# Kernel tuning notes

Measured on AMD Instinct MI355X. Metric: run time of the kernel, lower is better.

The kernel has to match this reference:

```python
import jax, jax.numpy as jnp
import numpy as np

EPS = 1e-8

def div_safe(n, d):
    return n / jnp.maximum(d, EPS)

def cos_sim(v1, v2):
    # torch F.cosine_similarity along last axis (broadcasting allowed)
    n1 = jnp.linalg.norm(v1, axis=-1)
    n2 = jnp.linalg.norm(v2, axis=-1)
    dot = jnp.sum(v1 * v2, axis=-1)
    return dot / (jnp.maximum(n1, EPS) * jnp.maximum(n2, EPS))

def cosine_pairwise(v1, v2):
    # v1: (B,L1,H), v2: (B,L2,H) -> (B,L1,L2)
    n1 = jnp.linalg.norm(v1, axis=2)[:, :, None]        # (B,L1,1)
    n2 = jnp.linalg.norm(v2, axis=2)[:, None, :]        # (B,1,L2)
    a = jnp.einsum('bih,bjh->bij', v1, v2)
    return div_safe(a, n1 * n2)

def mpm(v1, v2, w):
    # v1: (B,L,H); v2: (B,L,H) or (B,1,H) (broadcast); w: (P,H)
    mv1 = cos_sim(v1, v2)[..., None]                     # (B,L,1)
    v1w = w[None, None] * v1[:, :, None, :]              # (B,L,P,H)
    v2w = w[None, None] * v2[:, :, None, :]              # (B,L or 1,P,H)
    mvp = cos_sim(v1w, v2w)                              # (B,L,P)
    return [mv1, mvp]

def mpm_pairwise(v1, v2, w):
    # v1: (B,L1,H), v2: (B,L2,H), w: (P,H) -> (B,L1,L2,P)
    v1w = w[None, :, None, :] * v1[:, None, :, :]        # (B,P,L1,H)
    v2w = w[None, :, None, :] * v2[:, None, :, :]        # (B,P,L2,H)
    n = jnp.einsum('bpih,bpjh->bpij', v1w, v2w)
    n1 = jnp.linalg.norm(v1w, axis=3)[:, :, :, None]     # (B,P,L1,1)
    n2 = jnp.linalg.norm(v2w, axis=3)[:, :, None, :]     # (B,P,1,L2)
    return div_safe(n, n1 * n2).transpose(0, 2, 3, 1)

def matching_forward(context_p, mask_p, context_h, mask_h, params):
    H = params.shape[-1]
    B = context_p.shape[0]
    p_fw, p_bw = context_p[..., :H], context_p[..., H:]
    h_fw, h_bw = context_h[..., :H], context_h[..., H:]

    len_p = jnp.sum(mask_p, axis=1)
    len_h = jnp.sum(mask_h, axis=1)
    last_p = jnp.clip(len_p - 1, 0)
    last_h = jnp.clip(len_h - 1, 0)
    bidx = jnp.arange(B)
    p_fw_last = p_fw[bidx, last_p][:, None, :]           # (B,1,H)
    h_fw_last = h_fw[bidx, last_h][:, None, :]
    p_bw_last = p_bw[:, 0:1, :]
    h_bw_last = h_bw[:, 0:1, :]

    cos_fw = cosine_pairwise(p_fw, h_fw)                 # (B,L1,L2)
    cos_bw = cosine_pairwise(p_bw, h_bw)

    mv_p = [cos_fw.max(axis=2, keepdims=True), cos_fw.mean(axis=2, keepdims=True),
            cos_bw.max(axis=2, keepdims=True), cos_bw.mean(axis=2, keepdims=True)]
    mv_h = [cos_fw.max(axis=1)[..., None], cos_fw.mean(axis=1)[..., None],
            cos_bw.max(axis=1)[..., None], cos_bw.mean(axis=1)[..., None]]

    # full match
    mv_p += mpm(p_fw, h_fw_last, params[0]) + mpm(p_bw, h_bw_last, params[1])
    mv_h += mpm(h_fw, p_fw_last, params[0]) + mpm(h_bw, p_bw_last, params[1])

    # maxpool match
    m_fw = mpm_pairwise(p_fw, h_fw, params[2])           # (B,L1,L2,P)
    m_bw = mpm_pairwise(p_bw, h_bw, params[3])
    mv_p += [m_fw.max(axis=2), m_fw.mean(axis=2), m_bw.max(axis=2), m_bw.mean(axis=2)]
    mv_h += [m_fw.max(axis=1), m_fw.mean(axis=1), m_bw.max(axis=1), m_bw.mean(axis=1)]

    # attentive (mean) match -- sum over seq axis expressed as einsum, no 4D tensor
    att_mean_h_fw = div_safe(jnp.einsum('bij,bjh->bih', cos_fw, h_fw), cos_fw.sum(axis=2, keepdims=True))
    att_mean_h_bw = div_safe(jnp.einsum('bij,bjh->bih', cos_bw, h_bw), cos_bw.sum(axis=2, keepdims=True))
    att_mean_p_fw = div_safe(jnp.einsum('bij,bih->bjh', cos_fw, p_fw), cos_fw.sum(axis=1)[..., None])
    att_mean_p_bw = div_safe(jnp.einsum('bij,bih->bjh', cos_bw, p_bw), cos_bw.sum(axis=1)[..., None])
    mv_p += mpm(p_fw, att_mean_h_fw, params[4]) + mpm(p_bw, att_mean_h_bw, params[5])
    mv_h += mpm(h_fw, att_mean_p_fw, params[4]) + mpm(h_bw, att_mean_p_bw, params[5])

    # max-attentive match -- needs elementwise max over the pair axis
    att_max_h_fw = jnp.max(h_fw[:, None, :, :] * cos_fw[..., None], axis=2)  # (B,L1,H)
    att_max_h_bw = jnp.max(h_bw[:, None, :, :] * cos_bw[..., None], axis=2)
    att_max_p_fw = jnp.max(p_fw[:, :, None, :] * cos_fw[..., None], axis=1)  # (B,L2,H)
    att_max_p_bw = jnp.max(p_bw[:, :, None, :] * cos_bw[..., None], axis=1)
    mv_p += mpm(p_fw, att_max_h_fw, params[6]) + mpm(p_bw, att_max_h_bw, params[7])
    mv_h += mpm(h_fw, att_max_p_fw, params[6]) + mpm(h_bw, att_max_p_bw, params[7])

    return jnp.concatenate(mv_p, axis=2), jnp.concatenate(mv_h, axis=2)

def setup_inputs() -> dict:
    key = jax.random.key(0)
    k1, k2, k3 = jax.random.split(key, 3)
    B, L, H, P, M = 16, 128, 100, 20, 8
    context_p = jax.random.normal(k1, (B, L, 2 * H), dtype=jnp.float32)
    context_h = jax.random.normal(k2, (B, L, 2 * H), dtype=jnp.float32)
    mask_p = jnp.ones((B, L), dtype=jnp.int32)
    mask_h = jnp.ones((B, L), dtype=jnp.int32)
    # kaiming_normal_ (fan_in=H): std = sqrt(2/H)
    params = jax.random.normal(k3, (M, P, H), dtype=jnp.float32) * np.sqrt(2.0 / H)
    return {"context_p": context_p, "mask_p": mask_p,
            "context_h": context_h, "mask_h": mask_h, "params": params}

def reference(context_p, mask_p, context_h, mask_h, params):
    return matching_forward(context_p, mask_p, context_h, mask_h, params)
```

## Files before the change

kernel.cpp:

```cpp
#include <hip/hip_runtime.h>
#include <math.h>

#define B 16
#define L 128
#define H 100
#define P 20
#define CH 210
#define EPSF 1e-8f
#define MAGIC 0x13579BDF

#define OFF_COS   0u
#define OFF_COST  524288u
#define OFF_FLAGS 1048576u

typedef __attribute__((ext_vector_type(8))) short bf16x8;
typedef __attribute__((ext_vector_type(4))) float f32x4;

__device__ inline unsigned short f2bf(float x) {
    union { float f; unsigned u; } c; c.f = x;
    unsigned r = c.u + 0x7fffu + ((c.u >> 16) & 1u);
    return (unsigned short)(r >> 16);
}

__global__ __launch_bounds__(256, 2) void fused_kernel(
    const float* __restrict__ ctx_p, const int* __restrict__ mask_p,
    const float* __restrict__ ctx_h, const int* __restrict__ mask_h,
    const float* __restrict__ params,
    float* __restrict__ cosbuf, float* __restrict__ cosT,
    int* __restrict__ flags, float* __restrict__ out)
{
    __shared__ __align__(16) char smem[59904];
    const int k = blockIdx.x, t = threadIdx.x;

    if (k < 672) {
        int b, dir, p;
        if (k < 32) { b = k & 15; dir = k >> 4; p = P; }
        else { int idx = k - 32; b = idx & 15; dir = (idx >> 4) & 1; p = idx >> 5; }

        short* sB     = (short*)smem;
        float* colred = (float*)(smem + 32768);
        float* nlds   = (float*)(smem + 32768 + 4096);

        for (int e = t; e < 2048; e += 256) {
            int cgi = e >> 8, kt = (e >> 6) & 3, qq = (e >> 4) & 3, rl2 = e & 15;
            int row = cgi*16 + rl2, kb = kt*32 + qq*8;
            float v[8];
#pragma unroll
            for (int j = 0; j < 8; ++j) v[j] = 0.f;
            const float* src = ctx_h + (size_t)(b*L + row)*(2*H) + dir*H;
            if (kb < H)     { float4 f = *(const float4*)(src + kb);     v[0]=f.x; v[1]=f.y; v[2]=f.z; v[3]=f.w; }
            if (kb + 4 < H) { float4 f = *(const float4*)(src + kb + 4); v[4]=f.x; v[5]=f.y; v[6]=f.z; v[7]=f.w; }
            bf16x8 pk;
#pragma unroll
            for (int j = 0; j < 8; ++j) pk[j] = (short)f2bf(v[j]);
            *(bf16x8*)&sB[e*8] = pk;
        }

        const float* prow = params + ((size_t)(2 + dir)*P + p)*H;

        const int w = t >> 6, lane = t & 63, q = lane >> 4, rl = lane & 15;
        bf16x8 af[2][4];
#pragma unroll
        for (int rgi = 0; rgi < 2; ++rgi) {
            int row = (w*2 + rgi)*16 + rl;
            const float* src = ctx_p + (size_t)(b*L + row)*(2*H) + dir*H;
#pragma unroll
            for (int kt = 0; kt < 4; ++kt) {
                int kb = kt*32 + q*8;
                float v[8];
#pragma unroll
                for (int j = 0; j < 8; ++j) v[j] = 0.f;
                if (p < P) {
                    if (kb < H) {
                        float4 f = *(const float4*)(src + kb);
                        float4 wv = *(const float4*)(prow + kb);
                        v[0]=f.x*wv.x*wv.x; v[1]=f.y*wv.y*wv.y; v[2]=f.z*wv.z*wv.z; v[3]=f.w*wv.w*wv.w;
                    }
                    if (kb + 4 < H) {
                        float4 f = *(const float4*)(src + kb + 4);
                        float4 wv = *(const float4*)(prow + kb + 4);
                        v[4]=f.x*wv.x*wv.x; v[5]=f.y*wv.y*wv.y; v[6]=f.z*wv.z*wv.z; v[7]=f.w*wv.w*wv.w;
                    }
                } else {
                    if (kb < H)     { float4 f = *(const float4*)(src + kb);     v[0]=f.x; v[1]=f.y; v[2]=f.z; v[3]=f.w; }
                    if (kb + 4 < H) { float4 f = *(const float4*)(src + kb + 4); v[4]=f.x; v[5]=f.y; v[6]=f.z; v[7]=f.w; }
                }
                bf16x8 pk;
#pragma unroll
                for (int j = 0; j < 8; ++j) pk[j] = (short)f2bf(v[j]);
                af[rgi][kt] = pk;
            }
        }

        {
            const int r = t & 127, sd = t >> 7;
            const float* nrow = (sd ? ctx_h : ctx_p) + (size_t)(b*L + r)*(2*H) + dir*H;
            float n2 = 0.f;
            if (p < P) {
                for (int g = 0; g < 25; ++g) {
                    float4 v = *(const float4*)(nrow + 4*g);
                    float4 wv = *(const float4*)(prow + 4*g);
                    n2 = fmaf(wv.x*wv.x, v.x*v.x, n2);
                    n2 = fmaf(wv.y*wv.y, v.y*v.y, n2);
                    n2 = fmaf(wv.z*wv.z, v.z*v.z, n2);
                    n2 = fmaf(wv.w*wv.w, v.w*v.w, n2);
                }
            } else {
                for (int g = 0; g < 25; ++g) {
                    float4 v = *(const float4*)(nrow + 4*g);
                    n2 = fmaf(v.x, v.x, n2); n2 = fmaf(v.y, v.y, n2);
                    n2 = fmaf(v.z, v.z, n2); n2 = fmaf(v.w, v.w, n2);
                }
            }
            nlds[sd*128 + r] = sqrtf(n2);
        }
        __syncthreads();

        f32x4 acc[2][8];
#pragma unroll
        for (int rgi = 0; rgi < 2; ++rgi)
#pragma unroll
            for (int cgi = 0; cgi < 8; ++cgi) acc[rgi][cgi] = (f32x4)0.f;
#pragma unroll
        for (int kt = 0; kt < 4; ++kt) {
#pragma unroll
            for (int cgi = 0; cgi < 8; ++cgi) {
                bf16x8 bfr = *(bf16x8*)&sB[((cgi*4 + kt)*64 + lane)*8];
                acc[0][cgi] = __builtin_amdgcn_mfma_f32_16x16x32_bf16(af[0][kt], bfr, acc[0][cgi], 0, 0, 0);
                acc[1][cgi] = __builtin_amdgcn_mfma_f32_16x16x32_bf16(af[1][kt], bfr, acc[1][cgi], 0, 0, 0);
            }
        }

        float na[2][4];
#pragma unroll
        for (int rgi = 0; rgi < 2; ++rgi)
#pragma unroll
            for (int r = 0; r < 4; ++r) na[rgi][r] = nlds[0*128 + (w*2 + rgi)*16 + q*4 + r];
        float nbv[8];
#pragma unroll
        for (int cgi = 0; cgi < 8; ++cgi) nbv[cgi] = nlds[1*128 + cgi*16 + rl];

        const bool iscos = (p == P);
        float* cosm  = cosbuf + (size_t)(dir*B + b)*16384;
        float* cosmT = cosT   + (size_t)(dir*B + b)*16384;

        int chmax, chmean;
        if (p < P) { chmax = (dir ? 86 : 46) + p; chmean = (dir ? 106 : 66) + p; }
        else       { chmax = dir*2;              chmean = dir*2 + 1; }

        float rowm[2][4], rows_[2][4], colm[8], cols_[8];
#pragma unroll
        for (int rgi = 0; rgi < 2; ++rgi)
#pragma unroll
            for (int r = 0; r < 4; ++r) { rowm[rgi][r] = -INFINITY; rows_[rgi][r] = 0.f; }
#pragma unroll
        for (int cgi = 0; cgi < 8; ++cgi) { colm[cgi] = -INFINITY; cols_[cgi] = 0.f; }

#pragma unroll
        for (int rgi = 0; rgi < 2; ++rgi) {
            int i0 = (w*2 + rgi)*16 + q*4;
#pragma unroll
            for (int cgi = 0; cgi < 8; ++cgi) {
                float m[4];
#pragma unroll
                for (int r = 0; r < 4; ++r) {
                    float d = fmaxf(na[rgi][r]*nbv[cgi], EPSF);
                    m[r] = acc[rgi][cgi][r] * __builtin_amdgcn_rcpf(d);
                    rowm[rgi][r] = fmaxf(rowm[rgi][r], m[r]);
                    rows_[rgi][r] += m[r];
                }
                float cM = fmaxf(fmaxf(m[0], m[1]), fmaxf(m[2], m[3]));
                colm[cgi] = fmaxf(colm[cgi], cM);
                cols_[cgi] += (m[0] + m[1]) + (m[2] + m[3]);
                if (iscos) {
                    int j = cgi*16 + rl;
                    float4 f4; f4.x = m[0]; f4.y = m[1]; f4.z = m[2]; f4.w = m[3];
                    *(float4*)&cosmT[j*128 + i0] = f4;
#pragma unroll
                    for (int r = 0; r < 4; ++r) cosm[(i0 + r)*128 + j] = m[r];
                }
            }
        }
#pragma unroll
        for (int rgi = 0; rgi < 2; ++rgi)
#pragma unroll
            for (int r = 0; r < 4; ++r) {
                float mx = rowm[rgi][r], sm = rows_[rgi][r];
#pragma unroll
                for (int d = 1; d < 16; d <<= 1) {
                    mx = fmaxf(mx, __shfl_xor(mx, d));
                    sm += __shfl_xor(sm, d);
                }
                if (rl == 0) {
                    int i = (w*2 + rgi)*16 + q*4 + r;
                    float* orow = out + (size_t)(b*L + i)*CH;
                    orow[chmax] = mx; orow[chmean] = sm * (1.f/L);
                }
            }
#pragma unroll
        for (int cgi = 0; cgi < 8; ++cgi) {
            float mx = colm[cgi], sm = cols_[cgi];
            mx = fmaxf(mx, __shfl_xor(mx, 16)); sm += __shfl_xor(sm, 16);
            mx = fmaxf(mx, __shfl_xor(mx, 32)); sm += __shfl_xor(sm, 32);
            if (q == 0) {
                colred[(0*4 + w)*128 + cgi*16 + rl] = mx;
                colred[(1*4 + w)*128 + cgi*16 + rl] = sm;
            }
        }
        if (iscos) __threadfence();
        __syncthreads();
        if (iscos && t == 0)
            __hip_atomic_store(&flags[dir*16 + b], (int)MAGIC,
                               __ATOMIC_RELEASE, __HIP_MEMORY_SCOPE_AGENT);
        {
            int c = t & 127, kind = t >> 7;
            float v0 = colred[(kind*4 + 0)*128 + c], v1 = colred[(kind*4 + 1)*128 + c];
            float v2 = colred[(kind*4 + 2)*128 + c], v3 = colred[(kind*4 + 3)*128 + c];
            float* oh = out + (size_t)B*L*CH + (size_t)(b*L + c)*CH;
            if (kind == 0) {
                oh[chmax] = fmaxf(fmaxf(v0, v1), fmaxf(v2, v3));
            } else {
                float sm = (v0 + v1) + (v2 + v3);
                oh[chmean] = sm * (1.f/L);
            }
        }
        return;
    }

    if (k < 1184) {
        const int idx = k - 672;
        const int b = idx & 15, side = (idx >> 4) & 1, dir = (idx >> 5) & 1, rc = idx >> 6;
        const int r0 = rc*16;
        float* sf = (float*)smem;
        float (*sv)[100] = (float(*)[100])smem;
        float (*cvT)[16] = (float(*)[16])(smem + 51200);
        float (*denred)[16] = (float(*)[16])(smem + 59392);

        const float* mat = (side ? cosbuf : cosT) + (size_t)(dir*B + b)*16384;
        const float* srcJ = side ? ctx_p : ctx_h;
        const float* srcI = side ? ctx_h : ctx_p;

        for (int e = t; e < 3200; e += 256) {
            int row = e / 25, g = e - row*25;
            *(float4*)&sv[row][4*g] =
                *(const float4*)(srcJ + (size_t)(b*L + row)*(2*H) + dir*H + 4*g);
        }
        if (t == 0) {
            while (__hip_atomic_load(&flags[dir*16 + b],
                                     __ATOMIC_ACQUIRE, __HIP_MEMORY_SCOPE_AGENT) != (int)MAGIC)
                __builtin_amdgcn_s_sleep(2);
        }
        __syncthreads();

        for (int e = t; e < 2048; e += 256) {
            int s = e >> 4, r = e & 15;
            cvT[s][r] = mat[s*L + r0 + r];
        }
        __syncthreads();

        if (t < 128) {
            int row = t & 15, grp = t >> 4;
            float s = 0.f;
            for (int ss = 0; ss < 16; ++ss) s += cvT[grp*16 + ss][row];
            denred[grp][row] = s;
        }

        const int tr = t & 7, th = t >> 3;
        float acc[2][4], amx[2][4];
#pragma unroll
        for (int rr = 0; rr < 2; ++rr)
#pragma unroll
            for (int qq = 0; qq < 4; ++qq) { acc[rr][qq] = 0.f; amx[rr][qq] = -INFINITY; }
        if (th < 25) {
            for (int s = 0; s < L; ++s) {
                float2 c2 = *(const float2*)&cvT[s][2*tr];
                float4 v4 = *(const float4*)&sv[s][4*th];
                float cs[2] = {c2.x, c2.y};
                float vs[4] = {v4.x, v4.y, v4.z, v4.w};
#pragma unroll
                for (int rr = 0; rr < 2; ++rr)
#pragma unroll
                    for (int qq = 0; qq < 4; ++qq) {
                        float pr = cs[rr] * vs[qq];
                        acc[rr][qq] += pr;
                        amx[rr][qq] = fmaxf(amx[rr][qq], pr);
                    }
            }
        }
        __syncthreads();

        float* attv = sf;
        float* v1s  = sf + 3200;
        float* w2l  = sf + 4800;
        if (th < 25) {
#pragma unroll
            for (int rr = 0; rr < 2; ++rr) {
                int rloc = 2*tr + rr;
                float dsum = 0.f;
#pragma unroll
                for (int g = 0; g < 8; ++g) dsum += denred[g][rloc];
                float inv = 1.f / fmaxf(dsum, EPSF);
#pragma unroll
                for (int qq = 0; qq < 4; ++qq) {
                    attv[0*1600 + rloc*100 + 4*th + qq] = acc[rr][qq] * inv;
                    attv[1*1600 + rloc*100 + 4*th + qq] = amx[rr][qq];
                }
            }
        }
        for (int e = t; e < 400; e += 256) {
            int row = e / 25, g = e - row*25;
            *(float4*)&v1s[row*100 + 4*g] =
                *(const float4*)(srcI + (size_t)(b*L + r0 + row)*(2*H) + dir*H + 4*g);
        }
        for (int e = t; e < 4200; e += 256) {
            int kind = e >= 2100 ? 1 : 0, r = e - kind*2100;
            int h = r / 21, p = r - h*21;
            float v = 1.f;
            if (p < P) {
                float w = params[((size_t)((4 + kind*2 + dir)*P + p))*H + h];
                v = w*w;
            }
            w2l[kind*3600 + h*36 + p] = v;
        }
        __syncthreads();

        {
            const int task = t >> 3, tt = t & 7;
            const int kind = task >> 4, row = task & 15;
            const int h0 = tt*13, cnt = (tt < 7) ? 13 : 9;
            const float* av  = attv + kind*1600 + row*100;
            const float* v1r = v1s + row*100;
            const float* wk  = w2l + kind*3600;

            float s11[21], s22[21], s12[21];
#pragma unroll
            for (int p = 0; p < 21; ++p) { s11[p] = 0.f; s22[p] = 0.f; s12[p] = 0.f; }
            for (int hh = 0; hh < cnt; ++hh) {
                int h = h0 + hh;
                float a = v1r[h], c = av[h];
                float xx = a*a, yy = c*c, xy = a*c;
                const float* wrow = wk + h*36;
#pragma unroll
                for (int pg = 0; pg < 5; ++pg) {
                    float4 wv = *(const float4*)&wrow[4*pg];
                    float ws[4] = {wv.x, wv.y, wv.z, wv.w};
#pragma unroll
                    for (int q = 0; q < 4; ++q) {
                        int p = 4*pg + q;
                        s11[p] = fmaf(ws[q], xx, s11[p]);
                        s22[p] = fmaf(ws[q], yy, s22[p]);
                        s12[p] = fmaf(ws[q], xy, s12[p]);
                    }
                }
                float w20 = wrow[20];
                s11[20] = fmaf(w20, xx, s11[20]);
                s22[20] = fmaf(w20, yy, s22[20]);
                s12[20] = fmaf(w20, xy, s12[20]);
            }
#pragma unroll
            for (int p = 0; p < 21; ++p) {
#pragma unroll
                for (int d = 1; d < 8; d <<= 1) {
                    s11[p] += __shfl_xor(s11[p], d);
                    s22[p] += __shfl_xor(s22[p], d);
                    s12[p] += __shfl_xor(s12[p], d);
                }
            }
            if (tt == 0) {
                int chb = kind ? (dir ? 189 : 168) : (dir ? 147 : 126);
                float* orow = out + (size_t)side*B*L*CH + (size_t)(b*L + r0 + row)*CH;
#pragma unroll
                for (int p = 0; p < 21; ++p) {
                    float cv = s12[p] / (fmaxf(sqrtf(s11[p]), EPSF) * fmaxf(sqrtf(s22[p]), EPSF));
                    orow[(p == P) ? chb : (chb + 1 + p)] = cv;
                }
            }
        }
        return;
    }

    {
        const int idx = k - 1184;
        const int b = idx & 15, side = (idx >> 4) & 1, m = idx >> 5;
        const int i = t & 127, half = t >> 7;
        const int chb = m ? 25 : 4;
        const float* opp = side ? ctx_p : ctx_h;
        const int* omask = side ? mask_p : mask_h;

        int last = 0;
        if (m == 0) {
            int* sm = (int*)smem;
            if (t < 128) sm[t] = omask[b*L + t];
            __syncthreads();
            for (int s = 64; s > 0; s >>= 1) {
                if (t < s) sm[t] += sm[t + s];
                __syncthreads();
            }
            last = sm[0] - 1;
            if (last < 0) last = 0;
            __syncthreads();
        }

        const float* v1p = (side ? ctx_h : ctx_p) + (size_t)(b*L + i)*(2*H) + m*H;
        const float* v2p = (m == 0) ? (opp + (size_t)(b*L + last)*(2*H))
                                    : (opp + (size_t)(b*L + 0)*(2*H) + H);

        float s11[21], s22[21], s12[21];
#pragma unroll
        for (int p = 0; p < 21; ++p) { s11[p] = 0.f; s22[p] = 0.f; s12[p] = 0.f; }
        const int g0 = half ? 13 : 0, g1 = half ? 25 : 13;
        for (int g = g0; g < g1; ++g) {
            float4 x = *(const float4*)(v1p + 4*g);
            float4 y = *(const float4*)(v2p + 4*g);
            float xx[4] = {x.x*x.x, x.y*x.y, x.z*x.z, x.w*x.w};
            float yy[4] = {y.x*y.x, y.y*y.y, y.z*y.z, y.w*y.w};
            float xy[4] = {x.x*y.x, x.y*y.y, x.z*y.z, x.w*y.w};
#pragma unroll
            for (int hh = 0; hh < 4; ++hh) {
                int h = 4*g + hh;
#pragma unroll
                for (int p = 0; p < 21; ++p) {
                    float w2;
                    if (p < P) { float w = params[((size_t)(m*P + p))*H + h]; w2 = w*w; }
                    else w2 = 1.f;
                    s11[p] = fmaf(w2, xx[hh], s11[p]);
                    s22[p] = fmaf(w2, yy[hh], s22[p]);
                    s12[p] = fmaf(w2, xy[hh], s12[p]);
                }
            }
        }
        float* red = (float*)smem;
        if (half) {
#pragma unroll
            for (int p = 0; p < 21; ++p) {
                red[(0*21 + p)*128 + i] = s11[p];
                red[(1*21 + p)*128 + i] = s22[p];
                red[(2*21 + p)*128 + i] = s12[p];
            }
        }
        __syncthreads();
        if (!half) {
            float* orow = out + (size_t)side*B*L*CH + (size_t)(b*L + i)*CH;
#pragma unroll
            for (int p = 0; p < 21; ++p) {
                float a = s11[p] + red[(0*21 + p)*128 + i];
                float c = s22[p] + red[(1*21 + p)*128 + i];
                float d = s12[p] + red[(2*21 + p)*128 + i];
                float cv = d / (fmaxf(sqrtf(a), EPSF) * fmaxf(sqrtf(c), EPSF));
                orow[(p == P) ? chb : (chb + 1 + p)] = cv;
            }
        }
    }
}

extern "C" void kernel_launch(void* const* d_in, const int* in_sizes, int n_in,
                              void* d_out, int out_size, void* d_ws, size_t ws_size,
                              hipStream_t stream) {
    const float* ctx_p  = (const float*)d_in[0];
    const int*   mask_p = (const int*)d_in[1];
    const float* ctx_h  = (const float*)d_in[2];
    const int*   mask_h = (const int*)d_in[3];
    const float* params = (const float*)d_in[4];
    float* out = (float*)d_out;

    float* ws = (float*)d_ws;
    float* cosbuf = ws + OFF_COS;
    float* cosT   = ws + OFF_COST;
    int*   flags  = (int*)(ws + OFF_FLAGS);

    fused_kernel<<<dim3(1248), 256, 0, stream>>>(ctx_p, mask_p, ctx_h, mask_h, params,
                                                 cosbuf, cosT, flags, out);
}
```

Measured before the change: 121.7 us.

## Split fused kernel into two launches, dropping flag-based inter-block synchronization

The single persistent kernel, in which attention blocks spin on release/acquire flags set by cosine blocks, becomes two kernel launches: a pairwise matching kernel and an attentive/point matching kernel. Stream ordering takes over from the global flag handshake. Launch bounds rise to 4 blocks per SM with smaller LDS. The attentive-matching block is also restructured to stage context rows in two 64-row halves and to spread the 21 perspectives across 8 threads per row instead of shuffle reductions. The cost is an extra launch and the loss of overlap between the two phases.

New measurement: 122.0 us. No clear change (+0.2%).

```diff
diff --git a/kernel.cpp b/kernel.cpp
--- a/kernel.cpp
+++ b/kernel.cpp
@@ -7,11 +7,9 @@
 #define P 20
 #define CH 210
 #define EPSF 1e-8f
-#define MAGIC 0x13579BDF
 
 #define OFF_COS   0u
 #define OFF_COST  524288u
-#define OFF_FLAGS 1048576u
 
 typedef __attribute__((ext_vector_type(8))) short bf16x8;
 typedef __attribute__((ext_vector_type(4))) float f32x4;
@@ -22,365 +20,213 @@
     return (unsigned short)(r >> 16);
 }
 
-__global__ __launch_bounds__(256, 2) void fused_kernel(
+__global__ __launch_bounds__(256, 4) void pair_kernel(
+    const float* __restrict__ ctx_p, const float* __restrict__ ctx_h,
+    const float* __restrict__ params,
+    float* __restrict__ cosbuf, float* __restrict__ cosT,
+    float* __restrict__ out)
+{
+    __shared__ __align__(16) char smem[37888];
+    const int k = blockIdx.x, t = threadIdx.x;
+    const int b = k & 15, dir = (k >> 4) & 1, p = k >> 5;
+
+    short* sB     = (short*)smem;
+    float* colred = (float*)(smem + 32768);
+    float* nlds   = (float*)(smem + 32768 + 4096);
+
+    for (int e = t; e < 2048; e += 256) {
+        int cgi = e >> 8, kt = (e >> 6) & 3, qq = (e >> 4) & 3, rl2 = e & 15;
+        int row = cgi*16 + rl2, kb = kt*32 + qq*8;
+        float v[8];
+#pragma unroll
+        for (int j = 0; j < 8; ++j) v[j] = 0.f;
+        const float* src = ctx_h + (size_t)(b*L + row)*(2*H) + dir*H;
+        if (kb < H)     { float4 f = *(const float4*)(src + kb);     v[0]=f.x; v[1]=f.y; v[2]=f.z; v[3]=f.w; }
+        if (kb + 4 < H) { float4 f = *(const float4*)(src + kb + 4); v[4]=f.x; v[5]=f.y; v[6]=f.z; v[7]=f.w; }
+        bf16x8 pk;
+#pragma unroll
+        for (int j = 0; j < 8; ++j) pk[j] = (short)f2bf(v[j]);
+        *(bf16x8*)&sB[e*8] = pk;
+    }
+
+    const float* prow = params + ((size_t)(2 + dir)*P + p)*H;
+
+    const int w = t >> 6, lane = t & 63, q = lane >> 4, rl = lane & 15;
+    bf16x8 af[2][4];
+#pragma unroll
+    for (int rgi = 0; rgi < 2; ++rgi) {
+        int row = (w*2 + rgi)*16 + rl;
+        const float* src = ctx_p + (size_t)(b*L + row)*(2*H) + dir*H;
+#pragma unroll
+        for (int kt = 0; kt < 4; ++kt) {
+            int kb = kt*32 + q*8;
+            float v[8];
+#pragma unroll
+            for (int j = 0; j < 8; ++j) v[j] = 0.f;
+            if (p < P) {
+                if (kb < H) {
+                    float4 f = *(const float4*)(src + kb);
+                    float4 wv = *(const float4*)(prow + kb);
+                    v[0]=f.x*wv.x*wv.x; v[1]=f.y*wv.y*wv.y; v[2]=f.z*wv.z*wv.z; v[3]=f.w*wv.w*wv.w;
+                }
+                if (kb + 4 < H) {
+                    float4 f = *(const float4*)(src + kb + 4);
+                    float4 wv = *(const float4*)(prow + kb + 4);
+                    v[4]=f.x*wv.x*wv.x; v[5]=f.y*wv.y*wv.y; v[6]=f.z*wv.z*wv.z; v[7]=f.w*wv.w*wv.w;
+                }
+            } else {
+                if (kb < H)     { float4 f = *(const float4*)(src + kb);     v[0]=f.x; v[1]=f.y; v[2]=f.z; v[3]=f.w; }
+                if (kb + 4 < H) { float4 f = *(const float4*)(src + kb + 4); v[4]=f.x; v[5]=f.y; v[6]=f.z; v[7]=f.w; }
+            }
+            bf16x8 pk;
+#pragma unroll
+            for (int j = 0; j < 8; ++j) pk[j] = (short)f2bf(v[j]);
+            af[rgi][kt] = pk;
+        }
+    }
+
+    {
+        const int r = t & 127, sd = t >> 7;
+        const float* nrow = (sd ? ctx_h : ctx_p) + (size_t)(b*L + r)*(2*H) + dir*H;
+        float n2 = 0.f;
+        if (p < P) {
+            for (int g = 0; g < 25; ++g) {
+                float4 v = *(const float4*)(nrow + 4*g);
+                float4 wv = *(const float4*)(prow + 4*g);
+                n2 = fmaf(wv.x*wv.x, v.x*v.x, n2);
+                n2 = fmaf(wv.y*wv.y, v.y*v.y, n2);
+                n2 = fmaf(wv.z*wv.z, v.z*v.z, n2);
+                n2 = fmaf(wv.w*wv.w, v.w*v.w, n2);
+            }
+        } else {
+            for (int g = 0; g < 25; ++g) {
+                float4 v = *(const float4*)(nrow + 4*g);
+                n2 = fmaf(v.x, v.x, n2); n2 = fmaf(v.y, v.y, n2);
+                n2 = fmaf(v.z, v.z, n2); n2 = fmaf(v.w, v.w, n2);
+            }
+        }
+        nlds[sd*128 + r] = sqrtf(n2);
+    }
+    __syncthreads();
+
+    f32x4 acc[2][8];
+#pragma unroll
+    for (int rgi = 0; rgi < 2; ++rgi)
+#pragma unroll
+        for (int cgi = 0; cgi < 8; ++cgi) acc[rgi][cgi] = (f32x4)0.f;
+#pragma unroll
+    for (int kt = 0; kt < 4; ++kt) {
+#pragma unroll
+        for (int cgi = 0; cgi < 8; ++cgi) {
+            bf16x8 bfr = *(bf16x8*)&sB[((cgi*4 + kt)*64 + lane)*8];
+            acc[0][cgi] = __builtin_amdgcn_mfma_f32_16x16x32_bf16(af[0][kt], bfr, acc[0][cgi], 0, 0, 0);
+            acc[1][cgi] = __builtin_amdgcn_mfma_f32_16x16x32_bf16(af[1][kt], bfr, acc[1][cgi], 0, 0, 0);
+        }
+    }
+
+    float na[2][4];
+#pragma unroll
+    for (int rgi = 0; rgi < 2; ++rgi)
+#pragma unroll
+        for (int r = 0; r < 4; ++r) na[rgi][r] = nlds[0*128 + (w*2 + rgi)*16 + q*4 + r];
+    float nbv[8];
+#pragma unroll
+    for (int cgi = 0; cgi < 8; ++cgi) nbv[cgi] = nlds[1*128 + cgi*16 + rl];
+
+    const bool iscos = (p == P);
+    float* cosm  = cosbuf + (size_t)(dir*B + b)*16384;
+    float* cosmT = cosT   + (size_t)(dir*B + b)*16384;
+
+    int chmax, chmean;
+    if (p < P) { chmax = (dir ? 86 : 46) + p; chmean = (dir ? 106 : 66) + p; }
+    else       { chmax = dir*2;              chmean = dir*2 + 1; }
+
+    float rowm[2][4], rows_[2][4], colm[8], cols_[8];
+#pragma unroll
+    for (int rgi = 0; rgi < 2; ++rgi)
+#pragma unroll
+        for (int r = 0; r < 4; ++r) { rowm[rgi][r] = -INFINITY; rows_[rgi][r] = 0.f; }
+#pragma unroll
+    for (int cgi = 0; cgi < 8; ++cgi) { colm[cgi] = -INFINITY; cols_[cgi] = 0.f; }
+
+#pragma unroll
+    for (int rgi = 0; rgi < 2; ++rgi) {
+        int i0 = (w*2 + rgi)*16 + q*4;
+#pragma unroll
+        for (int cgi = 0; cgi < 8; ++cgi) {
+            float m[4];
+#pragma unroll
+            for (int r = 0; r < 4; ++r) {
+                float d = fmaxf(na[rgi][r]*nbv[cgi], EPSF);
+                m[r] = acc[rgi][cgi][r] * __builtin_amdgcn_rcpf(d);
+                rowm[rgi][r] = fmaxf(rowm[rgi][r], m[r]);
+                rows_[rgi][r] += m[r];
+            }
+            float cM = fmaxf(fmaxf(m[0], m[1]), fmaxf(m[2], m[3]));
+            colm[cgi] = fmaxf(colm[cgi], cM);
+            cols_[cgi] += (m[0] + m[1]) + (m[2] + m[3]);
+            if (iscos) {
+                int j = cgi*16 + rl;
+                float4 f4; f4.x = m[0]; f4.y = m[1]; f4.z = m[2]; f4.w = m[3];
+                *(float4*)&cosmT[j*128 + i0] = f4;
+#pragma unroll
+                for (int r = 0; r < 4; ++r) cosm[(i0 + r)*128 + j] = m[r];
+            }
+        }
+    }
+#pragma unroll
+    for (int rgi = 0; rgi < 2; ++rgi)
+#pragma unroll
+        for (int r = 0; r < 4; ++r) {
+            float mx = rowm[rgi][r], sm = rows_[rgi][r];
+#pragma unroll
+            for (int d = 1; d < 16; d <<= 1) {
+                mx = fmaxf(mx, __shfl_xor(mx, d));
+                sm += __shfl_xor(sm, d);
+            }
+            if (rl == 0) {
+                int i = (w*2 + rgi)*16 + q*4 + r;
+                float* orow = out + (size_t)(b*L + i)*CH;
+                orow[chmax] = mx; orow[chmean] = sm * (1.f/L);
+            }
+        }
+#pragma unroll
+    for (int cgi = 0; cgi < 8; ++cgi) {
+        float mx = colm[cgi], sm = cols_[cgi];
+        mx = fmaxf(mx, __shfl_xor(mx, 16)); sm += __shfl_xor(sm, 16);
+        mx = fmaxf(mx, __shfl_xor(mx, 32)); sm += __shfl_xor(sm, 32);
+        if (q == 0) {
+            colred[(0*4 + w)*128 + cgi*16 + rl] = mx;
+            colred[(1*4 + w)*128 + cgi*16 + rl] = sm;
+        }
+    }
+    __syncthreads();
+    {
+        int c = t & 127, kind = t >> 7;
+        float v0 = colred[(kind*4 + 0)*128 + c], v1 = colred[(kind*4 + 1)*128 + c];
+        float v2 = colred[(kind*4 + 2)*128 + c], v3 = colred[(kind*4 + 3)*128 + c];
+        float* oh = out + (size_t)B*L*CH + (size_t)(b*L + c)*CH;
+        if (kind == 0) {
+            oh[chmax] = fmaxf(fmaxf(v0, v1), fmaxf(v2, v3));
+        } else {
+            float sm = (v0 + v1) + (v2 + v3);
+            oh[chmean] = sm * (1.f/L);
+        }
+    }
+}
+
+__global__ __launch_bounds__(256, 4) void attpoint_kernel(
     const float* __restrict__ ctx_p, const int* __restrict__ mask_p,
     const float* __restrict__ ctx_h, const int* __restrict__ mask_h,
     const float* __restrict__ params,
-    float* __restrict__ cosbuf, float* __restrict__ cosT,
-    int* __restrict__ flags, float* __restrict__ out)
+    const float* __restrict__ cosbuf, const float* __restrict__ cosT,
+    float* __restrict__ out)
 {
-    __shared__ __align__(16) char smem[59904];
+    __shared__ __align__(16) char smem[36512];
     const int k = blockIdx.x, t = threadIdx.x;
 
-    if (k < 672) {
-        int b, dir, p;
-        if (k < 32) { b = k & 15; dir = k >> 4; p = P; }
-        else { int idx = k - 32; b = idx & 15; dir = (idx >> 4) & 1; p = idx >> 5; }
-
-        short* sB     = (short*)smem;
-        float* colred = (float*)(smem + 32768);
-        float* nlds   = (float*)(smem + 32768 + 4096);
-
-        for (int e = t; e < 2048; e += 256) {
-            int cgi = e >> 8, kt = (e >> 6) & 3, qq = (e >> 4) & 3, rl2 = e & 15;
-            int row = cgi*16 + rl2, kb = kt*32 + qq*8;
-            float v[8];
-#pragma unroll
-            for (int j = 0; j < 8; ++j) v[j] = 0.f;
-            const float* src = ctx_h + (size_t)(b*L + row)*(2*H) + dir*H;
-            if (kb < H)     { float4 f = *(const float4*)(src + kb);     v[0]=f.x; v[1]=f.y; v[2]=f.z; v[3]=f.w; }
-            if (kb + 4 < H) { float4 f = *(const float4*)(src + kb + 4); v[4]=f.x; v[5]=f.y; v[6]=f.z; v[7]=f.w; }
-            bf16x8 pk;
-#pragma unroll
-            for (int j = 0; j < 8; ++j) pk[j] = (short)f2bf(v[j]);
-            *(bf16x8*)&sB[e*8] = pk;
-        }
-
-        const float* prow = params + ((size_t)(2 + dir)*P + p)*H;
-
-        const int w = t >> 6, lane = t & 63, q = lane >> 4, rl = lane & 15;
-        bf16x8 af[2][4];
-#pragma unroll
-        for (int rgi = 0; rgi < 2; ++rgi) {
-            int row = (w*2 + rgi)*16 + rl;
-            const float* src = ctx_p + (size_t)(b*L + row)*(2*H) + dir*H;
-#pragma unroll
-            for (int kt = 0; kt < 4; ++kt) {
-                int kb = kt*32 + q*8;
-                float v[8];
-#pragma unroll
-                for (int j = 0; j < 8; ++j) v[j] = 0.f;
-                if (p < P) {
-                    if (kb < H) {
-                        float4 f = *(const float4*)(src + kb);
-                        float4 wv = *(const float4*)(prow + kb);
-                        v[0]=f.x*wv.x*wv.x; v[1]=f.y*wv.y*wv.y; v[2]=f.z*wv.z*wv.z; v[3]=f.w*wv.w*wv.w;
-                    }
-                    if (kb + 4 < H) {
-                        float4 f = *(const float4*)(src + kb + 4);
-                        float4 wv = *(const float4*)(prow + kb + 4);
-                        v[4]=f.x*wv.x*wv.x; v[5]=f.y*wv.y*wv.y; v[6]=f.z*wv.z*wv.z; v[7]=f.w*wv.w*wv.w;
-                    }
-                } else {
-                    if (kb < H)     { float4 f = *(const float4*)(src + kb);     v[0]=f.x; v[1]=f.y; v[2]=f.z; v[3]=f.w; }
-                    if (kb + 4 < H) { float4 f = *(const float4*)(src + kb + 4); v[4]=f.x; v[5]=f.y; v[6]=f.z; v[7]=f.w; }
-                }
-                bf16x8 pk;
-#pragma unroll
-                for (int j = 0; j < 8; ++j) pk[j] = (short)f2bf(v[j]);
-                af[rgi][kt] = pk;
-            }
-        }
-
-        {
-            const int r = t & 127, sd = t >> 7;
-            const float* nrow = (sd ? ctx_h : ctx_p) + (size_t)(b*L + r)*(2*H) + dir*H;
-            float n2 = 0.f;
-            if (p < P) {
-                for (int g = 0; g < 25; ++g) {
-                    float4 v = *(const float4*)(nrow + 4*g);
-                    float4 wv = *(const float4*)(prow + 4*g);
-                    n2 = fmaf(wv.x*wv.x, v.x*v.x, n2);
-                    n2 = fmaf(wv.y*wv.y, v.y*v.y, n2);
-                    n2 = fmaf(wv.z*wv.z, v.z*v.z, n2);
-                    n2 = fmaf(wv.w*wv.w, v.w*v.w, n2);
-                }
-            } else {
-                for (int g = 0; g < 25; ++g) {
-                    float4 v = *(const float4*)(nrow + 4*g);
-                    n2 = fmaf(v.x, v.x, n2); n2 = fmaf(v.y, v.y, n2);
-                    n2 = fmaf(v.z, v.z, n2); n2 = fmaf(v.w, v.w, n2);
-                }
-            }
-            nlds[sd*128 + r] = sqrtf(n2);
-        }
-        __syncthreads();
-
-        f32x4 acc[2][8];
-#pragma unroll
-        for (int rgi = 0; rgi < 2; ++rgi)
-#pragma unroll
-            for (int cgi = 0; cgi < 8; ++cgi) acc[rgi][cgi] = (f32x4)0.f;
-#pragma unroll
-        for (int kt = 0; kt < 4; ++kt) {
-#pragma unroll
-            for (int cgi = 0; cgi < 8; ++cgi) {
-                bf16x8 bfr = *(bf16x8*)&sB[((cgi*4 + kt)*64 + lane)*8];
-                acc[0][cgi] = __builtin_amdgcn_mfma_f32_16x16x32_bf16(af[0][kt], bfr, acc[0][cgi], 0, 0, 0);
-                acc[1][cgi] = __builtin_amdgcn_mfma_f32_16x16x32_bf16(af[1][kt], bfr, acc[1][cgi], 0, 0, 0);
-            }
-        }
-
-        float na[2][4];
-#pragma unroll
-        for (int rgi = 0; rgi < 2; ++rgi)
-#pragma unroll
-            for (int r = 0; r < 4; ++r) na[rgi][r] = nlds[0*128 + (w*2 + rgi)*16 + q*4 + r];
-        float nbv[8];
-#pragma unroll
-        for (int cgi = 0; cgi < 8; ++cgi) nbv[cgi] = nlds[1*128 + cgi*16 + rl];
-
-        const bool iscos = (p == P);
-        float* cosm  = cosbuf + (size_t)(dir*B + b)*16384;
-        float* cosmT = cosT   + (size_t)(dir*B + b)*16384;
-
-        int chmax, chmean;
-        if (p < P) { chmax = (dir ? 86 : 46) + p; chmean = (dir ? 106 : 66) + p; }
-        else       { chmax = dir*2;              chmean = dir*2 + 1; }
-
-        float rowm[2][4], rows_[2][4], colm[8], cols_[8];
-#pragma unroll
-        for (int rgi = 0; rgi < 2; ++rgi)
-#pragma unroll
-            for (int r = 0; r < 4; ++r) { rowm[rgi][r] = -INFINITY; rows_[rgi][r] = 0.f; }
-#pragma unroll
-        for (int cgi = 0; cgi < 8; ++cgi) { colm[cgi] = -INFINITY; cols_[cgi] = 0.f; }
-
-#pragma unroll
-        for (int rgi = 0; rgi < 2; ++rgi) {
-            int i0 = (w*2 + rgi)*16 + q*4;
-#pragma unroll
-            for (int cgi = 0; cgi < 8; ++cgi) {
-                float m[4];
-#pragma unroll
-                for (int r = 0; r < 4; ++r) {
-                    float d = fmaxf(na[rgi][r]*nbv[cgi], EPSF);
-                    m[r] = acc[rgi][cgi][r] * __builtin_amdgcn_rcpf(d);
-                    rowm[rgi][r] = fmaxf(rowm[rgi][r], m[r]);
-                    rows_[rgi][r] += m[r];
-                }
-                float cM = fmaxf(fmaxf(m[0], m[1]), fmaxf(m[2], m[3]));
-                colm[cgi] = fmaxf(colm[cgi], cM);
-                cols_[cgi] += (m[0] + m[1]) + (m[2] + m[3]);
-                if (iscos) {
-                    int j = cgi*16 + rl;
-                    float4 f4; f4.x = m[0]; f4.y = m[1]; f4.z = m[2]; f4.w = m[3];
-                    *(float4*)&cosmT[j*128 + i0] = f4;
-#pragma unroll
-                    for (int r = 0; r < 4; ++r) cosm[(i0 + r)*128 + j] = m[r];
-                }
-            }
-        }
-#pragma unroll
-        for (int rgi = 0; rgi < 2; ++rgi)
-#pragma unroll
-            for (int r = 0; r < 4; ++r) {
-                float mx = rowm[rgi][r], sm = rows_[rgi][r];
-#pragma unroll
-                for (int d = 1; d < 16; d <<= 1) {
-                    mx = fmaxf(mx, __shfl_xor(mx, d));
-                    sm += __shfl_xor(sm, d);
-                }
-                if (rl == 0) {
-                    int i = (w*2 + rgi)*16 + q*4 + r;
-                    float* orow = out + (size_t)(b*L + i)*CH;
-                    orow[chmax] = mx; orow[chmean] = sm * (1.f/L);
-                }
-            }
-#pragma unroll
-        for (int cgi = 0; cgi < 8; ++cgi) {
-            float mx = colm[cgi], sm = cols_[cgi];
-            mx = fmaxf(mx, __shfl_xor(mx, 16)); sm += __shfl_xor(sm, 16);
-            mx = fmaxf(mx, __shfl_xor(mx, 32)); sm += __shfl_xor(sm, 32);
-            if (q == 0) {
-                colred[(0*4 + w)*128 + cgi*16 + rl] = mx;
-                colred[(1*4 + w)*128 + cgi*16 + rl] = sm;
-            }
-        }
-        if (iscos) __threadfence();
-        __syncthreads();
-        if (iscos && t == 0)
-            __hip_atomic_store(&flags[dir*16 + b], (int)MAGIC,
-                               __ATOMIC_RELEASE, __HIP_MEMORY_SCOPE_AGENT);
-        {
-            int c = t & 127, kind = t >> 7;
-            float v0 = colred[(kind*4 + 0)*128 + c], v1 = colred[(kind*4 + 1)*128 + c];
-            float v2 = colred[(kind*4 + 2)*128 + c], v3 = colred[(kind*4 + 3)*128 + c];
-            float* oh = out + (size_t)B*L*CH + (size_t)(b*L + c)*CH;
-            if (kind == 0) {
-                oh[chmax] = fmaxf(fmaxf(v0, v1), fmaxf(v2, v3));
-            } else {
-                float sm = (v0 + v1) + (v2 + v3);
-                oh[chmean] = sm * (1.f/L);
-            }
-        }
-        return;
-    }
-
-    if (k < 1184) {
-        const int idx = k - 672;
-        const int b = idx & 15, side = (idx >> 4) & 1, dir = (idx >> 5) & 1, rc = idx >> 6;
-        const int r0 = rc*16;
-        float* sf = (float*)smem;
-        float (*sv)[100] = (float(*)[100])smem;
-        float (*cvT)[16] = (float(*)[16])(smem + 51200);
-        float (*denred)[16] = (float(*)[16])(smem + 59392);
-
-        const float* mat = (side ? cosbuf : cosT) + (size_t)(dir*B + b)*16384;
-        const float* srcJ = side ? ctx_p : ctx_h;
-        const float* srcI = side ? ctx_h : ctx_p;
-
-        for (int e = t; e < 3200; e += 256) {
-            int row = e / 25, g = e - row*25;
-            *(float4*)&sv[row][4*g] =
-                *(const float4*)(srcJ + (size_t)(b*L + row)*(2*H) + dir*H + 4*g);
-        }
-        if (t == 0) {
-            while (__hip_atomic_load(&flags[dir*16 + b],
-                                     __ATOMIC_ACQUIRE, __HIP_MEMORY_SCOPE_AGENT) != (int)MAGIC)
-                __builtin_amdgcn_s_sleep(2);
-        }
-        __syncthreads();
-
-        for (int e = t; e < 2048; e += 256) {
-            int s = e >> 4, r = e & 15;
-            cvT[s][r] = mat[s*L + r0 + r];
-        }
-        __syncthreads();
-
-        if (t < 128) {
-            int row = t & 15, grp = t >> 4;
-            float s = 0.f;
-            for (int ss = 0; ss < 16; ++ss) s += cvT[grp*16 + ss][row];
-            denred[grp][row] = s;
-        }
-
-        const int tr = t & 7, th = t >> 3;
-        float acc[2][4], amx[2][4];
-#pragma unroll
-        for (int rr = 0; rr < 2; ++rr)
-#pragma unroll
-            for (int qq = 0; qq < 4; ++qq) { acc[rr][qq] = 0.f; amx[rr][qq] = -INFINITY; }
-        if (th < 25) {
-            for (int s = 0; s < L; ++s) {
-                float2 c2 = *(const float2*)&cvT[s][2*tr];
-                float4 v4 = *(const float4*)&sv[s][4*th];
-                float cs[2] = {c2.x, c2.y};
-                float vs[4] = {v4.x, v4.y, v4.z, v4.w};
-#pragma unroll
-                for (int rr = 0; rr < 2; ++rr)
-#pragma unroll
-                    for (int qq = 0; qq < 4; ++qq) {
-                        float pr = cs[rr] * vs[qq];
-                        acc[rr][qq] += pr;
-                        amx[rr][qq] = fmaxf(amx[rr][qq], pr);
-                    }
-            }
-        }
-        __syncthreads();
-
-        float* attv = sf;
-        float* v1s  = sf + 3200;
-        float* w2l  = sf + 4800;
-        if (th < 25) {
-#pragma unroll
-            for (int rr = 0; rr < 2; ++rr) {
-                int rloc = 2*tr + rr;
-                float dsum = 0.f;
-#pragma unroll
-                for (int g = 0; g < 8; ++g) dsum += denred[g][rloc];
-                float inv = 1.f / fmaxf(dsum, EPSF);
-#pragma unroll
-                for (int qq = 0; qq < 4; ++qq) {
-                    attv[0*1600 + rloc*100 + 4*th + qq] = acc[rr][qq] * inv;
-                    attv[1*1600 + rloc*100 + 4*th + qq] = amx[rr][qq];
-                }
-            }
-        }
-        for (int e = t; e < 400; e += 256) {
-            int row = e / 25, g = e - row*25;
-            *(float4*)&v1s[row*100 + 4*g] =
-                *(const float4*)(srcI + (size_t)(b*L + r0 + row)*(2*H) + dir*H + 4*g);
-        }
-        for (int e = t; e < 4200; e += 256) {
-            int kind = e >= 2100 ? 1 : 0, r = e - kind*2100;
-            int h = r / 21, p = r - h*21;
-            float v = 1.f;
-            if (p < P) {
-                float w = params[((size_t)((4 + kind*2 + dir)*P + p))*H + h];
-                v = w*w;
-            }
-            w2l[kind*3600 + h*36 + p] = v;
-        }
-        __syncthreads();
-
-        {
-            const int task = t >> 3, tt = t & 7;
-            const int kind = task >> 4, row = task & 15;
-            const int h0 = tt*13, cnt = (tt < 7) ? 13 : 9;
-            const float* av  = attv + kind*1600 + row*100;
-            const float* v1r = v1s + row*100;
-            const float* wk  = w2l + kind*3600;
-
-            float s11[21], s22[21], s12[21];
-#pragma unroll
-            for (int p = 0; p < 21; ++p) { s11[p] = 0.f; s22[p] = 0.f; s12[p] = 0.f; }
-            for (int hh = 0; hh < cnt; ++hh) {
-                int h = h0 + hh;
-                float a = v1r[h], c = av[h];
-                float xx = a*a, yy = c*c, xy = a*c;
-                const float* wrow = wk + h*36;
-#pragma unroll
-                for (int pg = 0; pg < 5; ++pg) {
-                    float4 wv = *(const float4*)&wrow[4*pg];
-                    float ws[4] = {wv.x, wv.y, wv.z, wv.w};
-#pragma unroll
-                    for (int q = 0; q < 4; ++q) {
-                        int p = 4*pg + q;
-                        s11[p] = fmaf(ws[q], xx, s11[p]);
-                        s22[p] = fmaf(ws[q], yy, s22[p]);
-                        s12[p] = fmaf(ws[q], xy, s12[p]);
-                    }
-                }
-                float w20 = wrow[20];
-                s11[20] = fmaf(w20, xx, s11[20]);
-                s22[20] = fmaf(w20, yy, s22[20]);
-                s12[20] = fmaf(w20, xy, s12[20]);
-            }
-#pragma unroll
-            for (int p = 0; p < 21; ++p) {
-#pragma unroll
-                for (int d = 1; d < 8; d <<= 1) {
-                    s11[p] += __shfl_xor(s11[p], d);
-                    s22[p] += __shfl_xor(s22[p], d);
-                    s12[p] += __shfl_xor(s12[p], d);
-                }
-            }
-            if (tt == 0) {
-                int chb = kind ? (dir ? 189 : 168) : (dir ? 147 : 126);
-                float* orow = out + (size_t)side*B*L*CH + (size_t)(b*L + r0 + row)*CH;
-#pragma unroll
-                for (int p = 0; p < 21; ++p) {
-                    float cv = s12[p] / (fmaxf(sqrtf(s11[p]), EPSF) * fmaxf(sqrtf(s22[p]), EPSF));
-                    orow[(p == P) ? chb : (chb + 1 + p)] = cv;
-                }
-            }
-        }
-        return;
-    }
-
-    {
-        const int idx = k - 1184;
+    if (k >= 512) {
+        const int idx = k - 512;
         const int b = idx & 15, side = (idx >> 4) & 1, m = idx >> 5;
         const int i = t & 127, half = t >> 7;
         const int chb = m ? 25 : 4;
@@ -448,6 +294,155 @@
                 float d = s12[p] + red[(2*21 + p)*128 + i];
                 float cv = d / (fmaxf(sqrtf(a), EPSF) * fmaxf(sqrtf(c), EPSF));
                 orow[(p == P) ? chb : (chb + 1 + p)] = cv;
+            }
+        }
+        return;
+    }
+
+    {
+        const int b = k & 15, side = (k >> 4) & 1, dir = (k >> 5) & 1, rc = k >> 6;
+        const int r0 = rc*16;
+        float* svf = (float*)smem;
+        float (*cvT)[16] = (float(*)[16])(smem + 25600);
+        float* denred = (float*)(smem + 36000);
+        float* attv = (float*)smem;
+        float* v1s  = (float*)(smem + 12800);
+        float* w2l  = (float*)(smem + 19200);
+
+        const float* mat = (side ? cosbuf : cosT) + (size_t)(dir*B + b)*16384;
+        const float* srcJ = side ? ctx_p : ctx_h;
+        const float* srcI = side ? ctx_h : ctx_p;
+
+        for (int e = t; e < 1600; e += 256) {
+            int row = e / 25, g = e - row*25;
+            *(float4*)&svf[row*100 + 4*g] =
+                *(const float4*)(srcJ + (size_t)(b*L + row)*(2*H) + dir*H + 4*g);
+        }
+        for (int e = t; e < 2048; e += 256) {
+            int s = e >> 4, r = e & 15;
+            cvT[s][r] = mat[s*L + r0 + r];
+        }
+        __syncthreads();
+
+        if (t < 128) {
+            int row = t & 15, grp = t >> 4;
+            float s = 0.f;
+            for (int ss = 0; ss < 16; ++ss) s += cvT[grp*16 + ss][row];
+            denred[grp*16 + row] = s;
+        }
+
+        const int tr = t & 7, th = t >> 3;
+        float acc[2][4], amx[2][4];
+#pragma unroll
+        for (int rr = 0; rr < 2; ++rr)
+#pragma unroll
+            for (int qq = 0; qq < 4; ++qq) { acc[rr][qq] = 0.f; amx[rr][qq] = -INFINITY; }
+        if (th < 25) {
+            for (int s = 0; s < 64; ++s) {
+                float2 c2 = *(const float2*)&cvT[s][2*tr];
+                float4 v4 = *(const float4*)&svf[s*100 + 4*th];
+                float cs[2] = {c2.x, c2.y};
+                float vs[4] = {v4.x, v4.y, v4.z, v4.w};
+#pragma unroll
+                for (int rr = 0; rr < 2; ++rr)
+#pragma unroll
+                    for (int qq = 0; qq < 4; ++qq) {
+                        float pr = cs[rr] * vs[qq];
+                        acc[rr][qq] += pr;
+                        amx[rr][qq] = fmaxf(amx[rr][qq], pr);
+                    }
+            }
+        }
+        __syncthreads();
+
+        for (int e = t; e < 1600; e += 256) {
+            int row = e / 25, g = e - row*25;
+            *(float4*)&svf[row*100 + 4*g] =
+                *(const float4*)(srcJ + (size_t)(b*L + 64 + row)*(2*H) + dir*H + 4*g);
+        }
+        __syncthreads();
+
+        if (th < 25) {
+            for (int s = 0; s < 64; ++s) {
+                float2 c2 = *(const float2*)&cvT[64 + s][2*tr];
+                float4 v4 = *(const float4*)&svf[s*100 + 4*th];
+                float cs[2] = {c2.x, c2.y};
+                float vs[4] = {v4.x, v4.y, v4.z, v4.w};
+#pragma unroll
+                for (int rr = 0; rr < 2; ++rr)
+#pragma unroll
+                    for (int qq = 0; qq < 4; ++qq) {
+                        float pr = cs[rr] * vs[qq];
+                        acc[rr][qq] += pr;
+                        amx[rr][qq] = fmaxf(amx[rr][qq], pr);
+                    }
+            }
+        }
+        __syncthreads();
+
+        if (th < 25) {
+#pragma unroll
+            for (int rr = 0; rr < 2; ++rr) {
+                int rloc = 2*tr + rr;
+                float dsum = 0.f;
+#pragma unroll
+                for (int g = 0; g < 8; ++g) dsum += denred[g*16 + rloc];
+                float inv = 1.f / fmaxf(dsum, EPSF);
+#pragma unroll
+                for (int qq = 0; qq < 4; ++qq) {
+                    attv[0*1600 + rloc*100 + 4*th + qq] = acc[rr][qq] * inv;
+                    attv[1*1600 + rloc*100 + 4*th + qq] = amx[rr][qq];
+                }
+            }
+        }
+        for (int e = t; e < 400; e += 256) {
+            int row = e / 25, g = e - row*25;
+            *(float4*)&v1s[row*100 + 4*g] =
+                *(const float4*)(srcI + (size_t)(b*L + r0 + row)*(2*H) + dir*H + 4*g);
+        }
+        for (int e = t; e < 4200; e += 256) {
+            int kind = e >= 2100 ? 1 : 0, r = e - kind*2100;
+            int p = r / 100, h = r - p*100;
+            float v = 1.f;
+            if (p < P) {
+                float w = params[((size_t)((4 + kind*2 + dir)*P + p))*H + h];
+                v = w*w;
+            }
+            w2l[kind*2100 + p*100 + h] = v;
+        }
+        __syncthreads();
+
+        {
+            const int task = t >> 3, tt = t & 7;
+            const int kind = task >> 4, row = task & 15;
+            const float* av  = attv + kind*1600 + row*100;
+            const float* v1r = v1s + row*100;
+            const float* wk  = w2l + kind*2100;
+            const int p0 = tt, p1 = tt + 8, p2 = tt + 16;
+
+            float s11[3], s22[3], s12[3];
+#pragma unroll
+            for (int j = 0; j < 3; ++j) { s11[j] = 0.f; s22[j] = 0.f; s12[j] = 0.f; }
+            for (int h = 0; h < H; ++h) {
+                float a = v1r[h], c = av[h];
+                float xx = a*a, yy = c*c, xy = a*c;
+                float w0 = wk[p0*100 + h];
+                float w1 = wk[p1*100 + h];
+                float w2 = wk[p2*100 + h];
+                s11[0] = fmaf(w0, xx, s11[0]); s22[0] = fmaf(w0, yy, s22[0]); s12[0] = fmaf(w0, xy, s12[0]);
+                s11[1] = fmaf(w1, xx, s11[1]); s22[1] = fmaf(w1, yy, s22[1]); s12[1] = fmaf(w1, xy, s12[1]);
+                s11[2] = fmaf(w2, xx, s11[2]); s22[2] = fmaf(w2, yy, s22[2]); s12[2] = fmaf(w2, xy, s12[2]);
+            }
+            int chb = kind ? (dir ? 189 : 168) : (dir ? 147 : 126);
+            float* orow = out + (size_t)side*B*L*CH + (size_t)(b*L + r0 + row)*CH;
+            int pown[3] = {p0, p1, p2};
+#pragma unroll
+            for (int j = 0; j < 3; ++j) {
+                int p = pown[j];
+                if (p < 21) {
+                    float cv = s12[j] / (fmaxf(sqrtf(s11[j]), EPSF) * fmaxf(sqrtf(s22[j]), EPSF));
+                    orow[(p == P) ? chb : (chb + 1 + p)] = cv;
+                }
             }
         }
     }
@@ -466,8 +461,9 @@
     float* ws = (float*)d_ws;
     float* cosbuf = ws + OFF_COS;
     float* cosT   = ws + OFF_COST;
-    int*   flags  = (int*)(ws + OFF_FLAGS);
-
-    fused_kernel<<<dim3(1248), 256, 0, stream>>>(ctx_p, mask_p, ctx_h, mask_h, params,
-                                                 cosbuf, cosT, flags, out);
+
+    pair_kernel    <<<dim3(672), 256, 0, stream>>>(ctx_p, ctx_h, params,
+                                                   cosbuf, cosT, out);
+    attpoint_kernel<<<dim3(576), 256, 0, stream>>>(ctx_p, mask_p, ctx_h, mask_h, params,
+                                                   cosbuf, cosT, out);
 }
```
